# Kernel tuning notes

Measured on AMD Instinct MI355X. Metric: run time of the kernel, lower is better.

The kernel has to match this reference:

```python
import jax, jax.numpy as jnp
import numpy as np

B, S, D = 2, 2048, 2048
H, KV, HD = 32, 8, 64  # num_heads, num_kv_heads, head_dim
NREP = H // KV


def rotate_half(x):
    x1, x2 = x[..., : x.shape[-1] // 2], x[..., x.shape[-1] // 2 :]
    return jnp.concatenate((-x2, x1), axis=-1)


def setup_inputs() -> dict:
    key = jax.random.key(0)
    ks = jax.random.split(key, 5)
    x = jax.random.normal(ks[0], (B, S, D), dtype=jnp.float32)
    # weights stored as [in, out] so y = x @ W (same math as nn.Linear with random init)
    Wq = jax.random.normal(ks[1], (D, D), dtype=jnp.float32) * (D ** -0.5)
    Wk = jax.random.normal(ks[2], (D, KV * HD), dtype=jnp.float32) * (D ** -0.5)
    Wv = jax.random.normal(ks[3], (D, KV * HD), dtype=jnp.float32) * (D ** -0.5)
    Wo = jax.random.normal(ks[4], (D, D), dtype=jnp.float32) * (D ** -0.5)
    # standard RoPE tables, broadcastable over [B, H, S, HD]
    inv_freq = 1.0 / (10000.0 ** (jnp.arange(0, HD, 2, dtype=jnp.float32) / HD))
    freqs = jnp.arange(S, dtype=jnp.float32)[:, None] * inv_freq[None, :]  # [S, HD/2]
    emb = jnp.concatenate((freqs, freqs), axis=-1)  # [S, HD]
    cos = jnp.cos(emb)[None, None]  # [1,1,S,HD]
    sin = jnp.sin(emb)[None, None]
    # causal mask, masked where == 0
    attention_mask = jnp.tril(jnp.ones((S, S), dtype=jnp.int32))[None, None]
    return {"x": x, "cos": cos, "sin": sin, "Wq": Wq, "Wk": Wk, "Wv": Wv,
            "Wo": Wo, "attention_mask": attention_mask}


def reference(x, cos, sin, Wq, Wk, Wv, Wo, attention_mask):
    b, s, _ = x.shape
    q = (x @ Wq).reshape(b, s, H, HD).transpose(0, 2, 1, 3)   # [B,H,S,HD]
    k = (x @ Wk).reshape(b, s, KV, HD).transpose(0, 2, 1, 3)  # [B,KV,S,HD]
    v = (x @ Wv).reshape(b, s, KV, HD).transpose(0, 2, 1, 3)  # [B,KV,S,HD]
    # RoPE (elementwise) commutes with head-repeat; apply before grouping
    q = q * cos + rotate_half(q) * sin
    k = k * cos + rotate_half(k) * sin
    # GQA head broadcast instead of repeat_interleave: group q as [B,KV,NREP,S,HD]
    qg = q.reshape(b, KV, NREP, s, HD)
    scores = jnp.einsum('bgrqd,bgkd->bgrqk', qg, k) / jnp.sqrt(jnp.float32(HD))
    scores = jnp.where(attention_mask[:, :, None] == 0, jnp.float32(-1e9), scores)
    probs = jax.nn.softmax(scores, axis=-1)
    out = jnp.einsum('bgrqk,bgkd->bgrqd', probs, v)           # [B,KV,NREP,S,HD]
    out = out.reshape(b, H, s, HD).transpose(0, 2, 1, 3).reshape(b, s, H * HD)
    return out @ Wo
```

## Files before the change

### kernel.cpp

```cpp
#include <hip/hip_runtime.h>
#include <hip/hip_bf16.h>
#include <stdint.h>

#define B_ 2
#define S_ 2048
#define D_ 2048
#define H_ 32
#define KV_ 8
#define HD_ 64
#define NQKV 3072

typedef __bf16 bf16_t;
typedef __bf16 bf16x8 __attribute__((ext_vector_type(8)));
typedef __bf16 bf16x4 __attribute__((ext_vector_type(4)));
typedef float  f32x4  __attribute__((ext_vector_type(4)));
typedef float  f32x16 __attribute__((ext_vector_type(16)));
typedef unsigned int u32;
typedef u32 u32x4 __attribute__((ext_vector_type(4)));

typedef const __attribute__((address_space(1))) uint32_t* gp1_t;
typedef __attribute__((address_space(3))) uint32_t* lp3_t;

__device__ inline void gload_lds16(const void* g, void* l) {
  __builtin_amdgcn_global_load_lds((gp1_t)(uintptr_t)g, (lp3_t)(uint32_t)(uintptr_t)l,
                                   16, 0, 0);
}

__device__ inline u32 pkbf(float a, float b) {
  union { bf16_t h[2]; u32 u; } v;
  v.h[0] = (bf16_t)a; v.h[1] = (bf16_t)b;
  return v.u;
}

__device__ inline void pl32swap(u32 &a, u32 &b) {
  asm("v_permlane32_swap_b32 %0, %1" : "+v"(a), "+v"(b));
}

__global__ void cvt_f32_bf16(const float* __restrict__ in, bf16_t* __restrict__ out, int n4) {
  int i = blockIdx.x * blockDim.x + threadIdx.x;
  if (i < n4) {
    float4 v = ((const float4*)in)[i];
    bf16x4 o;
    o[0] = (bf16_t)v.x; o[1] = (bf16_t)v.y; o[2] = (bf16_t)v.z; o[3] = (bf16_t)v.w;
    ((bf16x4*)out)[i] = o;
  }
}

__global__ void transpose_cvt(const float* __restrict__ in, bf16_t* __restrict__ out,
                              int C, int row_off) {
  __shared__ float t[32][33];
  int tx = threadIdx.x, ty = threadIdx.y;
  int c0 = blockIdx.x * 32, r0 = blockIdx.y * 32;
#pragma unroll
  for (int j = 0; j < 4; ++j)
    t[ty + j*8][tx] = in[(int64_t)(r0 + ty + j*8) * C + c0 + tx];
  __syncthreads();
#pragma unroll
  for (int j = 0; j < 4; ++j)
    out[(int64_t)(row_off + c0 + ty + j*8) * 2048 + r0 + tx] = (bf16_t)t[tx][ty + j*8];
}

__global__ void v_transpose(const bf16_t* __restrict__ Vbuf, bf16_t* __restrict__ Vt) {
  __shared__ bf16_t t[32][34];
  const int tx = threadIdx.x, ty = threadIdx.y;
  const int c0 = blockIdx.x * 32;
  const int s0 = blockIdx.y * 32;
  const int b  = blockIdx.z;
#pragma unroll
  for (int j = 0; j < 4; ++j)
    t[ty + j*8][tx] = Vbuf[(int64_t)(b * S_ + s0 + ty + j*8) * 512 + c0 + tx];
  __syncthreads();
#pragma unroll
  for (int j = 0; j < 4; ++j)
    Vt[(int64_t)(b * 512 + c0 + ty + j*8) * S_ + s0 + tx] = t[tx][ty + j*8];
}

#define QSCALE 0.18033688011112042f
template <int BN, int EPI>
__global__ __launch_bounds__(512, 2) void gemm256(const bf16_t* __restrict__ A,
                                                  const bf16_t* __restrict__ Bt,
                                                  const float* __restrict__ cosb,
                                                  const float* __restrict__ sinb,
                                                  bf16_t* __restrict__ Q,
                                                  bf16_t* __restrict__ Kr,
                                                  bf16_t* __restrict__ Vbuf,
                                                  float* __restrict__ Cout,
                                                  int N, int K) {
  constexpr int NB = BN / 64;
  constexpr int LT = 4 + NB;
  constexpr int WCOLS = BN / 4;
  constexpr int NF = WCOLS / 16;

  __shared__ bf16_t As[2][256 * 64];
  __shared__ bf16_t Bs[2][BN * 64];

  const int tid = threadIdx.x;
  const int w = tid >> 6, lane = tid & 63;
  const int l15 = lane & 15, l4 = lane >> 4;
  const int wr = w >> 2, wc = w & 3;
  const int bm = blockIdx.y * 256, bn = blockIdx.x * BN;

  const int rw = w * 8 + (lane >> 3);
  const int srcg = ((lane & 7) ^ ((lane >> 3) & 7)) << 3;
  const bf16_t* PA[4];
  const bf16_t* PB[NB];
#pragma unroll
  for (int L = 0; L < 4; ++L)
    PA[L] = A + (int64_t)(bm + L * 64 + rw) * K + srcg;
#pragma unroll
  for (int L = 0; L < NB; ++L)
    PB[L] = Bt + (int64_t)(bn + L * 64 + rw) * K + srcg;

  const int NK = K >> 6;
  const int xr = l15 & 7;
  const int g0 = (l4 ^ xr) << 3;
  const int g1 = ((4 + l4) ^ xr) << 3;

  f32x4 acc[8][NF] = {};

#pragma unroll
  for (int s = 0; s < LT; ++s) {
    if (s < 4) gload_lds16(PA[s], &As[0][s * 4096 + w * 512]);
    else       gload_lds16(PB[s - 4], &Bs[0][(s - 4) * 4096 + w * 512]);
  }
  asm volatile("s_waitcnt vmcnt(0)" ::: "memory");
  __syncthreads();

  for (int t = 0; t < NK; ++t) {
    const int p = t & 1;
    const bool more = (t + 1) < NK;
    const int toff = (t + 1) << 6;
    const bf16_t* Ab = &As[p][0];
    const bf16_t* Bb = &Bs[p][0];

    bf16x8 ball[NF][2];
#pragma unroll
    for (int nn = 0; nn < NF; ++nn) {
      const int rb = wc * WCOLS + nn * 16 + l15;
      ball[nn][0] = *(const bf16x8*)(Bb + rb * 64 + g0);
      ball[nn][1] = *(const bf16x8*)(Bb + rb * 64 + g1);
    }

#pragma unroll
    for (int mh = 0; mh < 2; ++mh) {
      if (more) {
        const int s0 = mh * (LT / 2), s1 = s0 + LT / 2;
#pragma unroll
        for (int s = s0; s < s1; ++s) {
          if (s < 4) gload_lds16(PA[s] + toff, &As[p ^ 1][s * 4096 + w * 512]);
          else       gload_lds16(PB[s - 4] + toff, &Bs[p ^ 1][(s - 4) * 4096 + w * 512]);
        }
      }
      bf16x8 af[4][2];
#pragma unroll
      for (int mm = 0; mm < 4; ++mm) {
        const int ra = wr * 128 + (mh * 4 + mm) * 16 + l15;
        af[mm][0] = *(const bf16x8*)(Ab + ra * 64 + g0);
        af[mm][1] = *(const bf16x8*)(Ab + ra * 64 + g1);
      }
      __builtin_amdgcn_s_setprio(1);
#pragma unroll
      for (int mm = 0; mm < 4; ++mm)
#pragma unroll
        for (int nn = 0; nn < NF; ++nn) {
          acc[mh*4+mm][nn] = __builtin_amdgcn_mfma_f32_16x16x32_bf16(
              af[mm][0], ball[nn][0], acc[mh*4+mm][nn], 0, 0, 0);
          acc[mh*4+mm][nn] = __builtin_amdgcn_mfma_f32_16x16x32_bf16(
              af[mm][1], ball[nn][1], acc[mh*4+mm][nn], 0, 0, 0);
        }
      __builtin_amdgcn_s_setprio(0);
    }
    if (more) {
      asm volatile("s_waitcnt vmcnt(0)" ::: "memory");
      __syncthreads();
    }
  }

  if constexpr (EPI == 0) {
#pragma unroll
    for (int m = 0; m < 8; ++m) {
      const int row = bm + wr * 128 + m * 16 + l4 * 4;
#pragma unroll
      for (int n = 0; n < NF; ++n) {
        const int col = bn + wc * WCOLS + n * 16 + l15;
#pragma unroll
        for (int r = 0; r < 4; ++r)
          Cout[(int64_t)(row + r) * N + col] = acc[m][n][r];
      }
    }
  } else {
    const int colbase = bn + wc * 64;
    if (colbase < 2048) {
      const int h = colbase >> 6;
#pragma unroll
      for (int m = 0; m < 8; ++m) {
#pragma unroll
        for (int r = 0; r < 4; ++r) {
          const int srow = bm + wr * 128 + m * 16 + l4 * 4 + r;
          const int b = srow >> 11, s = srow & 2047;
          const float* cs = cosb + s * HD_;
          const float* sn = sinb + s * HD_;
          bf16_t* qp = Q + ((int64_t)(b * H_ + h) * S_ + s) * HD_;
#pragma unroll
          for (int n = 0; n < 4; ++n) {
            const int d = n * 16 + l15;
            const float sgn = (n & 2) ? 1.f : -1.f;
            float o = (acc[m][n][r] * cs[d] + sgn * acc[m][n ^ 2][r] * sn[d]) * QSCALE;
            qp[d] = (bf16_t)o;
          }
        }
      }
    } else if (colbase < 2560) {
      const int kvh = (colbase - 2048) >> 6;
#pragma unroll
      for (int m = 0; m < 8; ++m) {
#pragma unroll
        for (int r = 0; r < 4; ++r) {
          const int srow = bm + wr * 128 + m * 16 + l4 * 4 + r;
          const int b = srow >> 11, s = srow & 2047;
          const float* cs = cosb + s * HD_;
          const float* sn = sinb + s * HD_;
          bf16_t* kp = Kr + ((int64_t)(b * KV_ + kvh) * S_ + s) * HD_;
#pragma unroll
          for (int n = 0; n < 4; ++n) {
            const int d = n * 16 + l15;
            const float sgn = (n & 2) ? 1.f : -1.f;
            float o = acc[m][n][r] * cs[d] + sgn * acc[m][n ^ 2][r] * sn[d];
            kp[d] = (bf16_t)o;
          }
        }
      }
    } else {
      const int ccb = colbase - 2560;
#pragma unroll
      for (int m = 0; m < 8; ++m) {
#pragma unroll
        for (int r = 0; r < 4; ++r) {
          const int srow = bm + wr * 128 + m * 16 + l4 * 4 + r;
          bf16_t* vp = Vbuf + (int64_t)srow * 512 + ccb;
#pragma unroll
          for (int n = 0; n < 4; ++n)
            vp[n * 16 + l15] = (bf16_t)acc[m][n][r];
        }
      }
    }
  }
}

#define SHIFT_ 8.0f
__global__ __launch_bounds__(512) void attn6(const bf16_t* __restrict__ Q,
                                             const bf16_t* __restrict__ Kr,
                                             const bf16_t* __restrict__ Vt,
                                             bf16_t* __restrict__ AO) {
  const int bk = blockIdx.x;
  const int b = bk >> 3, kvh = bk & 7;
  const int qc = 31 - (int)blockIdx.y;
  const int tid = threadIdx.x;
  const int w = tid >> 6, lane = tid & 63;
  const int l31 = lane & 31, hi = lane >> 5;
  const int h = kvh * 4 + (w & 3);
  const int q0w = qc * 64 + (w >> 2) * 32;

  __shared__ __align__(16) bf16_t Ks[3][64 * 64];
  __shared__ __align__(16) bf16_t Vs[3][64 * 64];

  const bf16_t* Qb = Q  + ((int64_t)(b * H_ + h) * S_ + q0w) * HD_;
  const bf16_t* Kg = Kr + (int64_t)(b * KV_ + kvh) * S_ * HD_;
  const bf16_t* Vg = Vt + (int64_t)(b * KV_ + kvh) * HD_ * S_;

  const int rL = (w << 3) + (lane >> 3);
  const int sgr = ((lane & 7) ^ (rL & 7)) << 3;
  const bf16_t* Ksrc = Kg + rL * HD_ + sgr;
  const bf16_t* Vsrc = Vg + (int64_t)rL * S_ + sgr;
  char* KsDst = (char*)&Ks[0][0] + w * 1024;
  char* VsDst = (char*)&Vs[0][0] + w * 1024;

  const int NT = qc + 1;

  auto stage = [&](int t) {
    const int tc = (t < NT) ? t : (NT - 1);
    const int bufo = (t % 3) * 8192;
    gload_lds16(Ksrc + tc * 64 * HD_, KsDst + bufo);
    gload_lds16(Vsrc + tc * 64,      VsDst + bufo);
  };

  bf16x8 qf[4];
#pragma unroll
  for (int ds = 0; ds < 4; ++ds)
    qf[ds] = *(const bf16x8*)(Qb + l31 * HD_ + ds * 16 + hi * 8);

  f32x16 accO0 = {}, accO1 = {};
  float lhalf = 0.f;
  const int xorb = l31 & 7;

  const char* KsB = (const char*)&Ks[0][0];
  const char* VsB = (const char*)&Vs[0][0];

  const f32x16 sinit = {SHIFT_ > 0 ? -SHIFT_ : 0.f, -SHIFT_, -SHIFT_, -SHIFT_,
                        -SHIFT_, -SHIFT_, -SHIFT_, -SHIFT_,
                        -SHIFT_, -SHIFT_, -SHIFT_, -SHIFT_,
                        -SHIFT_, -SHIFT_, -SHIFT_, -SHIFT_};

  stage(0);
  stage(1);

  for (int t = 0; t < NT; ++t) {
    asm volatile("s_waitcnt vmcnt(2)" ::: "memory");
    __syncthreads();
    stage(t + 2);
    const int curo = (t % 3) * 8192;
#pragma unroll
    for (int sub = 0; sub < 2; ++sub) {
      const int kvbase = t * 64 + sub * 32;
      if (kvbase <= q0w) {
        const bool diag = (kvbase == q0w);
        const char* Kbase = KsB + curo + (sub * 32 + l31) * 128;
        f32x16 sacc = sinit;
        __builtin_amdgcn_s_setprio(1);
#pragma unroll
        for (int ds = 0; ds < 4; ++ds) {
          bf16x8 kf = *(const bf16x8*)(Kbase + ((((ds << 1) + hi) ^ xorb) << 4));
          sacc = __builtin_amdgcn_mfma_f32_32x32x16_bf16(kf, qf[ds], sacc, 0, 0, 0);
        }
        __builtin_amdgcn_s_setprio(0);
        float p[16];
#pragma unroll
        for (int r = 0; r < 16; ++r) {
          float sc = sacc[r];
          if (diag) {
            int kvpos = (r & 3) + 8 * (r >> 2) + 4 * hi;
            if (kvpos > l31) sc = -1e30f;
          }
          p[r] = __builtin_amdgcn_exp2f(sc);
        }
        float t0 = (p[0] + p[1]) + (p[2] + p[3]);
        float t1 = (p[4] + p[5]) + (p[6] + p[7]);
        float t2 = (p[8] + p[9]) + (p[10] + p[11]);
        float t3 = (p[12] + p[13]) + (p[14] + p[15]);
        lhalf += (t0 + t1) + (t2 + t3);
        u32 pk[8];
#pragma unroll
        for (int i = 0; i < 8; ++i) pk[i] = pkbf(p[2*i], p[2*i+1]);
        u32 a0 = pk[0], b0 = pk[2]; pl32swap(a0, b0);
        u32 a1 = pk[1], b1 = pk[3]; pl32swap(a1, b1);
        u32 a2 = pk[4], b2 = pk[6]; pl32swap(a2, b2);
        u32 a3 = pk[5], b3 = pk[7]; pl32swap(a3, b3);
        bf16x8 pf0 = __builtin_bit_cast(bf16x8, (u32x4){a0, a1, b0, b1});
        bf16x8 pf1 = __builtin_bit_cast(bf16x8, (u32x4){a2, a3, b2, b3});
        const char* Vb0 = VsB + curo + l31 * 128;
        const char* Vb1 = VsB + curo + (32 + l31) * 128;
        const int c0 = (sub << 2) + hi;
        const int c1 = (sub << 2) + 2 + hi;
        bf16x8 v00 = *(const bf16x8*)(Vb0 + ((c0 ^ xorb) << 4));
        bf16x8 v01 = *(const bf16x8*)(Vb0 + ((c1 ^ xorb) << 4));
        bf16x8 v10 = *(const bf16x8*)(Vb1 + ((c0 ^ xorb) << 4));
        bf16x8 v11 = *(const bf16x8*)(Vb1 + ((c1 ^ xorb) << 4));
        __builtin_amdgcn_s_setprio(1);
        accO0 = __builtin_amdgcn_mfma_f32_32x32x16_bf16(v00, pf0, accO0, 0, 0, 0);
        accO1 = __builtin_amdgcn_mfma_f32_32x32x16_bf16(v10, pf0, accO1, 0, 0, 0);
        accO0 = __builtin_amdgcn_mfma_f32_32x32x16_bf16(v01, pf1, accO0, 0, 0, 0);
        accO1 = __builtin_amdgcn_mfma_f32_32x32x16_bf16(v11, pf1, accO1, 0, 0, 0);
        __builtin_amdgcn_s_setprio(0);
      }
    }
  }

  asm volatile("s_waitcnt vmcnt(0)" ::: "memory");

  float lrun = lhalf + __shfl_xor(lhalf, 32);
  const float rl = 1.f / lrun;
  const int64_t row = (int64_t)(b * S_ + q0w + l31);
#pragma unroll
  for (int dt = 0; dt < 2; ++dt) {
#pragma unroll
    for (int g = 0; g < 4; ++g) {
      bf16x4 ov;
#pragma unroll
      for (int j = 0; j < 4; ++j) {
        float val = (dt ? accO1[4*g + j] : accO0[4*g + j]) * rl;
        ov[j] = (bf16_t)val;
      }
      const int d0 = dt * 32 + g * 8 + hi * 4;
      *(bf16x4*)(AO + row * D_ + h * HD_ + d0) = ov;
    }
  }
}

extern "C" void kernel_launch(void* const* d_in, const int* in_sizes, int n_in,
                              void* d_out, int out_size, void* d_ws, size_t ws_size,
                              hipStream_t stream) {
  const float* x    = (const float*)d_in[0];
  const float* cosb = (const float*)d_in[1];
  const float* sinb = (const float*)d_in[2];
  const float* Wq   = (const float*)d_in[3];
  const float* Wk   = (const float*)d_in[4];
  const float* Wv   = (const float*)d_in[5];
  const float* Wo   = (const float*)d_in[6];
  float* out = (float*)d_out;

  bf16_t* ws = (bf16_t*)d_ws;
  size_t o = 0;
  bf16_t* xb    = ws + o; o += (size_t)4096 * 2048;
  bf16_t* Wqkvt = ws + o; o += (size_t)3072 * 2048;
  bf16_t* Wot   = ws + o; o += (size_t)2048 * 2048;
  bf16_t* Qr    = ws + o; o += (size_t)B_ * H_ * S_ * HD_;
  bf16_t* Krb   = ws + o; o += (size_t)B_ * KV_ * S_ * HD_;
  bf16_t* Vtb   = ws + o; o += (size_t)B_ * KV_ * S_ * HD_;
  bf16_t* Vbuf  = ws + o; o += (size_t)B_ * S_ * 512;
  bf16_t* AO    = ws + o; o += (size_t)4096 * 2048;

  cvt_f32_bf16<<<(8388608/4 + 255)/256, 256, 0, stream>>>(x, xb, 8388608/4);
  transpose_cvt<<<dim3(2048/32, 2048/32), dim3(32, 8), 0, stream>>>(Wq, Wqkvt, 2048, 0);
  transpose_cvt<<<dim3(512/32, 2048/32),  dim3(32, 8), 0, stream>>>(Wk, Wqkvt, 512, 2048);
  transpose_cvt<<<dim3(512/32, 2048/32),  dim3(32, 8), 0, stream>>>(Wv, Wqkvt, 512, 2560);
  transpose_cvt<<<dim3(2048/32, 2048/32), dim3(32, 8), 0, stream>>>(Wo, Wot, 2048, 0);
  gemm256<256, 1><<<dim3(3072/256, 4096/256), 512, 0, stream>>>(
      xb, Wqkvt, cosb, sinb, Qr, Krb, Vbuf, nullptr, 3072, 2048);
  v_transpose<<<dim3(16, 64, 2), dim3(32, 8), 0, stream>>>(Vbuf, Vtb);
  attn6<<<dim3(16, 32), 512, 0, stream>>>(Qr, Krb, Vtb, AO);
  gemm256<128, 0><<<dim3(2048/128, 4096/256), 512, 0, stream>>>(
      AO, Wot, nullptr, nullptr, nullptr, nullptr, nullptr, out, 2048, 2048);
}
```

Measured before the change: 187.2 us.

## Pair mirrored causal query tiles per wave to balance attention work

The attention kernel now uses 256-thread blocks where each wave handles two 32-row query tiles, one near the start and its mirror near the end of the sequence. Every block then does roughly the same causal work, and each K fragment read from LDS feeds two QK^T MFMA chains. This removes the load imbalance of the old reversed-chunk scheduling, where blocks differed widely in length. In exchange each wave holds twice the Q fragments and accumulators, raising register pressure, and each thread issues twice as many LDS-staging loads per tile.

```diff
diff --git a/kernel.cpp b/kernel.cpp
--- a/kernel.cpp
+++ b/kernel.cpp
@@ -248,118 +248,140 @@
 }
 
 #define SHIFT_ 8.0f
-__global__ __launch_bounds__(512) void attn6(const bf16_t* __restrict__ Q,
-                                             const bf16_t* __restrict__ Kr,
-                                             const bf16_t* __restrict__ Vt,
-                                             bf16_t* __restrict__ AO) {
+__global__ __launch_bounds__(256, 2) void attn7(const bf16_t* __restrict__ Q,
+                                                const bf16_t* __restrict__ Kr,
+                                                const bf16_t* __restrict__ Vt,
+                                                bf16_t* __restrict__ AO) {
   const int bk = blockIdx.x;
   const int b = bk >> 3, kvh = bk & 7;
-  const int qc = 31 - (int)blockIdx.y;
+  const int y = blockIdx.y;
+  const int q0A = y * 32, q0B = (63 - y) * 32;
   const int tid = threadIdx.x;
   const int w = tid >> 6, lane = tid & 63;
   const int l31 = lane & 31, hi = lane >> 5;
-  const int h = kvh * 4 + (w & 3);
-  const int q0w = qc * 64 + (w >> 2) * 32;
+  const int h = kvh * 4 + w;
 
   __shared__ __align__(16) bf16_t Ks[3][64 * 64];
   __shared__ __align__(16) bf16_t Vs[3][64 * 64];
 
-  const bf16_t* Qb = Q  + ((int64_t)(b * H_ + h) * S_ + q0w) * HD_;
   const bf16_t* Kg = Kr + (int64_t)(b * KV_ + kvh) * S_ * HD_;
   const bf16_t* Vg = Vt + (int64_t)(b * KV_ + kvh) * HD_ * S_;
 
   const int rL = (w << 3) + (lane >> 3);
   const int sgr = ((lane & 7) ^ (rL & 7)) << 3;
-  const bf16_t* Ksrc = Kg + rL * HD_ + sgr;
+  const bf16_t* Ksrc = Kg + (int64_t)rL * HD_ + sgr;
   const bf16_t* Vsrc = Vg + (int64_t)rL * S_ + sgr;
-  char* KsDst = (char*)&Ks[0][0] + w * 1024;
-  char* VsDst = (char*)&Vs[0][0] + w * 1024;
-
-  const int NT = qc + 1;
+
+  const int NT = (63 - y) / 2 + 1;
 
   auto stage = [&](int t) {
     const int tc = (t < NT) ? t : (NT - 1);
-    const int bufo = (t % 3) * 8192;
-    gload_lds16(Ksrc + tc * 64 * HD_, KsDst + bufo);
-    gload_lds16(Vsrc + tc * 64,      VsDst + bufo);
+    char* Kd = (char*)Ks + (t % 3) * 8192 + w * 1024;
+    char* Vd = (char*)Vs + (t % 3) * 8192 + w * 1024;
+    gload_lds16(Ksrc + (int64_t)tc * 64 * HD_, Kd);
+    gload_lds16(Ksrc + (int64_t)(tc * 64 + 32) * HD_, Kd + 4096);
+    gload_lds16(Vsrc + tc * 64, Vd);
+    gload_lds16(Vsrc + (int64_t)32 * S_ + tc * 64, Vd + 4096);
   };
 
-  bf16x8 qf[4];
-#pragma unroll
-  for (int ds = 0; ds < 4; ++ds)
-    qf[ds] = *(const bf16x8*)(Qb + l31 * HD_ + ds * 16 + hi * 8);
-
-  f32x16 accO0 = {}, accO1 = {};
-  float lhalf = 0.f;
+  const bf16_t* QbA = Q + ((int64_t)(b * H_ + h) * S_ + q0A) * HD_;
+  const bf16_t* QbB = Q + ((int64_t)(b * H_ + h) * S_ + q0B) * HD_;
+  bf16x8 qfA[4], qfB[4];
+#pragma unroll
+  for (int ds = 0; ds < 4; ++ds) {
+    qfA[ds] = *(const bf16x8*)(QbA + l31 * HD_ + ds * 16 + hi * 8);
+    qfB[ds] = *(const bf16x8*)(QbB + l31 * HD_ + ds * 16 + hi * 8);
+  }
+
+  f32x16 aA0 = {}, aA1 = {}, aB0 = {}, aB1 = {};
+  float lhA = 0.f, lhB = 0.f;
   const int xorb = l31 & 7;
 
-  const char* KsB = (const char*)&Ks[0][0];
-  const char* VsB = (const char*)&Vs[0][0];
-
-  const f32x16 sinit = {SHIFT_ > 0 ? -SHIFT_ : 0.f, -SHIFT_, -SHIFT_, -SHIFT_,
+  const f32x16 sinit = {-SHIFT_, -SHIFT_, -SHIFT_, -SHIFT_,
                         -SHIFT_, -SHIFT_, -SHIFT_, -SHIFT_,
                         -SHIFT_, -SHIFT_, -SHIFT_, -SHIFT_,
                         -SHIFT_, -SHIFT_, -SHIFT_, -SHIFT_};
 
+  auto softmax_pack = [&](const f32x16 &sacc, bool diag, float &lh,
+                          bf16x8 &pf0, bf16x8 &pf1) {
+    float p[16];
+#pragma unroll
+    for (int r = 0; r < 16; ++r) {
+      float sc = sacc[r];
+      if (diag) {
+        int kvpos = (r & 3) + 8 * (r >> 2) + 4 * hi;
+        if (kvpos > l31) sc = -1e30f;
+      }
+      p[r] = __builtin_amdgcn_exp2f(sc);
+    }
+    float t0 = (p[0] + p[1]) + (p[2] + p[3]);
+    float t1 = (p[4] + p[5]) + (p[6] + p[7]);
+    float t2 = (p[8] + p[9]) + (p[10] + p[11]);
+    float t3 = (p[12] + p[13]) + (p[14] + p[15]);
+    lh += (t0 + t1) + (t2 + t3);
+    u32 pk[8];
+#pragma unroll
+    for (int i = 0; i < 8; ++i) pk[i] = pkbf(p[2*i], p[2*i+1]);
+    u32 a0 = pk[0], b0 = pk[2]; pl32swap(a0, b0);
+    u32 a1 = pk[1], b1 = pk[3]; pl32swap(a1, b1);
+    u32 a2 = pk[4], b2 = pk[6]; pl32swap(a2, b2);
+    u32 a3 = pk[5], b3 = pk[7]; pl32swap(a3, b3);
+    pf0 = __builtin_bit_cast(bf16x8, (u32x4){a0, a1, b0, b1});
+    pf1 = __builtin_bit_cast(bf16x8, (u32x4){a2, a3, b2, b3});
+  };
+
   stage(0);
   stage(1);
 
   for (int t = 0; t < NT; ++t) {
-    asm volatile("s_waitcnt vmcnt(2)" ::: "memory");
+    asm volatile("s_waitcnt vmcnt(4)" ::: "memory");
     __syncthreads();
     stage(t + 2);
-    const int curo = (t % 3) * 8192;
+    const char* KsB = (const char*)Ks + (t % 3) * 8192;
+    const char* VsB = (const char*)Vs + (t % 3) * 8192;
 #pragma unroll
     for (int sub = 0; sub < 2; ++sub) {
       const int kvbase = t * 64 + sub * 32;
-      if (kvbase <= q0w) {
-        const bool diag = (kvbase == q0w);
-        const char* Kbase = KsB + curo + (sub * 32 + l31) * 128;
-        f32x16 sacc = sinit;
+      if (kvbase <= q0B) {
+        const bool actA = (kvbase <= q0A);
+        const char* Kbase = KsB + (sub * 32 + l31) * 128;
+        bf16x8 kf[4];
+#pragma unroll
+        for (int ds = 0; ds < 4; ++ds)
+          kf[ds] = *(const bf16x8*)(Kbase + ((((ds << 1) + hi) ^ xorb) << 4));
+        f32x16 sA = sinit, sB = sinit;
         __builtin_amdgcn_s_setprio(1);
 #pragma unroll
-        for (int ds = 0; ds < 4; ++ds) {
-          bf16x8 kf = *(const bf16x8*)(Kbase + ((((ds << 1) + hi) ^ xorb) << 4));
-          sacc = __builtin_amdgcn_mfma_f32_32x32x16_bf16(kf, qf[ds], sacc, 0, 0, 0);
+        for (int ds = 0; ds < 4; ++ds)
+          sB = __builtin_amdgcn_mfma_f32_32x32x16_bf16(kf[ds], qfB[ds], sB, 0, 0, 0);
+        if (actA) {
+#pragma unroll
+          for (int ds = 0; ds < 4; ++ds)
+            sA = __builtin_amdgcn_mfma_f32_32x32x16_bf16(kf[ds], qfA[ds], sA, 0, 0, 0);
         }
         __builtin_amdgcn_s_setprio(0);
-        float p[16];
-#pragma unroll
-        for (int r = 0; r < 16; ++r) {
-          float sc = sacc[r];
-          if (diag) {
-            int kvpos = (r & 3) + 8 * (r >> 2) + 4 * hi;
-            if (kvpos > l31) sc = -1e30f;
-          }
-          p[r] = __builtin_amdgcn_exp2f(sc);
-        }
-        float t0 = (p[0] + p[1]) + (p[2] + p[3]);
-        float t1 = (p[4] + p[5]) + (p[6] + p[7]);
-        float t2 = (p[8] + p[9]) + (p[10] + p[11]);
-        float t3 = (p[12] + p[13]) + (p[14] + p[15]);
-        lhalf += (t0 + t1) + (t2 + t3);
-        u32 pk[8];
-#pragma unroll
-        for (int i = 0; i < 8; ++i) pk[i] = pkbf(p[2*i], p[2*i+1]);
-        u32 a0 = pk[0], b0 = pk[2]; pl32swap(a0, b0);
-        u32 a1 = pk[1], b1 = pk[3]; pl32swap(a1, b1);
-        u32 a2 = pk[4], b2 = pk[6]; pl32swap(a2, b2);
-        u32 a3 = pk[5], b3 = pk[7]; pl32swap(a3, b3);
-        bf16x8 pf0 = __builtin_bit_cast(bf16x8, (u32x4){a0, a1, b0, b1});
-        bf16x8 pf1 = __builtin_bit_cast(bf16x8, (u32x4){a2, a3, b2, b3});
-        const char* Vb0 = VsB + curo + l31 * 128;
-        const char* Vb1 = VsB + curo + (32 + l31) * 128;
+        bf16x8 pA0, pA1, pB0, pB1;
+        softmax_pack(sB, kvbase == q0B, lhB, pB0, pB1);
+        if (actA) softmax_pack(sA, kvbase == q0A, lhA, pA0, pA1);
+        const char* Vb0 = VsB + l31 * 128;
+        const char* Vb1 = VsB + (32 + l31) * 128;
         const int c0 = (sub << 2) + hi;
-        const int c1 = (sub << 2) + 2 + hi;
+        const int c1 = c0 + 2;
         bf16x8 v00 = *(const bf16x8*)(Vb0 + ((c0 ^ xorb) << 4));
         bf16x8 v01 = *(const bf16x8*)(Vb0 + ((c1 ^ xorb) << 4));
         bf16x8 v10 = *(const bf16x8*)(Vb1 + ((c0 ^ xorb) << 4));
         bf16x8 v11 = *(const bf16x8*)(Vb1 + ((c1 ^ xorb) << 4));
         __builtin_amdgcn_s_setprio(1);
-        accO0 = __builtin_amdgcn_mfma_f32_32x32x16_bf16(v00, pf0, accO0, 0, 0, 0);
-        accO1 = __builtin_amdgcn_mfma_f32_32x32x16_bf16(v10, pf0, accO1, 0, 0, 0);
-        accO0 = __builtin_amdgcn_mfma_f32_32x32x16_bf16(v01, pf1, accO0, 0, 0, 0);
-        accO1 = __builtin_amdgcn_mfma_f32_32x32x16_bf16(v11, pf1, accO1, 0, 0, 0);
+        aB0 = __builtin_amdgcn_mfma_f32_32x32x16_bf16(v00, pB0, aB0, 0, 0, 0);
+        aB1 = __builtin_amdgcn_mfma_f32_32x32x16_bf16(v10, pB0, aB1, 0, 0, 0);
+        aB0 = __builtin_amdgcn_mfma_f32_32x32x16_bf16(v01, pB1, aB0, 0, 0, 0);
+        aB1 = __builtin_amdgcn_mfma_f32_32x32x16_bf16(v11, pB1, aB1, 0, 0, 0);
+        if (actA) {
+          aA0 = __builtin_amdgcn_mfma_f32_32x32x16_bf16(v00, pA0, aA0, 0, 0, 0);
+          aA1 = __builtin_amdgcn_mfma_f32_32x32x16_bf16(v10, pA0, aA1, 0, 0, 0);
+          aA0 = __builtin_amdgcn_mfma_f32_32x32x16_bf16(v01, pA1, aA0, 0, 0, 0);
+          aA1 = __builtin_amdgcn_mfma_f32_32x32x16_bf16(v11, pA1, aA1, 0, 0, 0);
+        }
         __builtin_amdgcn_s_setprio(0);
       }
     }
@@ -367,23 +389,27 @@
 
   asm volatile("s_waitcnt vmcnt(0)" ::: "memory");
 
-  float lrun = lhalf + __shfl_xor(lhalf, 32);
-  const float rl = 1.f / lrun;
-  const int64_t row = (int64_t)(b * S_ + q0w + l31);
-#pragma unroll
-  for (int dt = 0; dt < 2; ++dt) {
-#pragma unroll
-    for (int g = 0; g < 4; ++g) {
-      bf16x4 ov;
-#pragma unroll
-      for (int j = 0; j < 4; ++j) {
-        float val = (dt ? accO1[4*g + j] : accO0[4*g + j]) * rl;
-        ov[j] = (bf16_t)val;
-      }
-      const int d0 = dt * 32 + g * 8 + hi * 4;
-      *(bf16x4*)(AO + row * D_ + h * HD_ + d0) = ov;
-    }
-  }
+  auto epi = [&](const f32x16 &a0, const f32x16 &a1, float lh, int q0) {
+    float l = lh + __shfl_xor(lh, 32);
+    const float rl = 1.f / l;
+    const int64_t row = (int64_t)(b * S_ + q0 + l31);
+#pragma unroll
+    for (int dt = 0; dt < 2; ++dt) {
+#pragma unroll
+      for (int g = 0; g < 4; ++g) {
+        bf16x4 ov;
+#pragma unroll
+        for (int j = 0; j < 4; ++j) {
+          float val = (dt ? a1[4*g + j] : a0[4*g + j]) * rl;
+          ov[j] = (bf16_t)val;
+        }
+        const int d0 = dt * 32 + g * 8 + hi * 4;
+        *(bf16x4*)(AO + row * D_ + h * HD_ + d0) = ov;
+      }
+    }
+  };
+  epi(aA0, aA1, lhA, q0A);
+  epi(aB0, aB1, lhB, q0B);
 }
 
 extern "C" void kernel_launch(void* const* d_in, const int* in_sizes, int n_in,
@@ -417,7 +443,7 @@
   gemm256<256, 1><<<dim3(3072/256, 4096/256), 512, 0, stream>>>(
       xb, Wqkvt, cosb, sinb, Qr, Krb, Vbuf, nullptr, 3072, 2048);
   v_transpose<<<dim3(16, 64, 2), dim3(32, 8), 0, stream>>>(Vbuf, Vtb);
-  attn6<<<dim3(16, 32), 512, 0, stream>>>(Qr, Krb, Vtb, AO);
+  attn7<<<dim3(16, 32), 256, 0, stream>>>(Qr, Krb, Vtb, AO);
   gemm256<128, 0><<<dim3(2048/128, 4096/256), 512, 0, stream>>>(
       AO, Wot, nullptr, nullptr, nullptr, nullptr, nullptr, out, 2048, 2048);
 }
```

New measurement: 180.4 us. 3.6% less time.
